# Performance work log

Measured on AMD Instinct MI355X. Metric: run time of the kernel, lower is better.

The kernel has to match this reference:

```python
import jax, jax.numpy as jnp
import numpy as np

N = 1200          # number of mentions in the block -> NxN SDP matrix
HID = 128         # MLP hidden width
RANK = 64         # Burer-Monteiro factor rank ~ sqrt(2N)
SDP_ITERS = 100   # fixed iteration budget (original caps at 50000)
BN_EPS = 1e-5


def setup_inputs() -> dict:
    key = jax.random.key(0)
    k = jax.random.split(key, 5)
    P = N * (N - 1) // 2
    x = jax.random.normal(k[0], (P, 39), jnp.float32)
    W1 = jax.random.normal(k[1], (39, HID), jnp.float32) * (1.0 / np.sqrt(39.0))
    b1 = jnp.zeros((HID,), jnp.float32)
    gamma = jnp.ones((HID,), jnp.float32)
    beta = jnp.zeros((HID,), jnp.float32)
    W2 = jax.random.normal(k[2], (HID, 1), jnp.float32) * (1.0 / np.sqrt(float(HID)))
    b2 = jnp.zeros((1,), jnp.float32)
    V0 = jax.random.normal(k[3], (N, RANK), jnp.float32)
    return {"x": x, "W1": W1, "b1": b1, "gamma": gamma, "beta": beta,
            "W2": W2, "b2": b2, "V0": V0}


def _forward(x, W1, b1, gamma, beta, W2, b2, V0):
    # MLPLayer: Linear -> BatchNorm (batch stats) -> ReLU -> Linear(->1)
    h = x @ W1 + b1                                   # [P, HID]
    mu = h.mean(axis=0)
    var = h.var(axis=0)
    h = (h - mu) * jax.lax.rsqrt(var + BN_EPS) * gamma + beta
    h = jax.nn.relu(h)
    w = (h @ W2 + b2).reshape(-1)                     # flat edge weights [P]

    # UncompressTransformLayer: flat upper-triangle -> symmetric NxN, zero diag
    iu, ju = jnp.triu_indices(N, k=1)
    A = jnp.zeros((N, N), w.dtype).at[iu, ju].set(w)
    W = A + A.T                                       # [N, N]

    # SDPLayer: max <W, X> s.t. X PSD, diag(X)=1, X>=0 via Burer-Monteiro
    # low-rank factorization with fixed-iteration projected gradient ascent.
    V = V0 / jnp.linalg.norm(V0, axis=1, keepdims=True)
    lr = 1.0 / (jnp.linalg.norm(W) + 1e-8)

    def step(V, _):
        V = V + lr * (W @ V)
        V = V / jnp.linalg.norm(V, axis=1, keepdims=True)
        return V, None

    V, _ = jax.lax.scan(step, V, None, length=SDP_ITERS)
    X = jnp.clip(V @ V.T, 0.0, 1.0)                   # output probabilities [N, N]
    return X


def reference(x, W1, b1, gamma, beta, W2, b2, V0):
    return _forward(x, W1, b1, gamma, beta, W2, b2, V0)
```

## Files before the change

kernel.cpp:

```cpp
#include <hip/hip_runtime.h>

#define NM 1200
#define PP 719400
#define HID 128
#define RANK 64
#define SDP_ITERS 100

#define OFF_S      0
#define OFF_SUMW2  1600
#define OFF_CVEC   1664
#define OFF_W1S    1792
#define OFF_WVEC   6912
#define OFF_WMAT   726400
#define OFF_VA     2166400
#define OFF_VB     2243200

__device__ __forceinline__ float wave_reduce_sum(float v) {
#pragma unroll
    for (int o = 32; o > 0; o >>= 1) v += __shfl_xor(v, o, 64);
    return v;
}

__global__ __launch_bounds__(256) void zero_kernel(float* __restrict__ ws, int n) {
    int i = blockIdx.x * 256 + threadIdx.x;
    if (i < n) ws[i] = 0.0f;
}

#define STATS_BLOCKS 1024
#define KT 40
__global__ __launch_bounds__(256) void stats_kernel(const float* __restrict__ x,
                                                    float* __restrict__ S) {
    __shared__ __align__(16) float tile[2][KT * 48];
    __shared__ float Sacc[48 * 48];
    const int tid = threadIdx.x;
    for (int i = tid; i < 48 * 48; i += 256) Sacc[i] = 0.f;
    for (int i = tid; i < 2 * KT * 8; i += 256) {
        int b = i / (KT * 8);
        int rem = i - b * (KT * 8);
        int r = rem >> 3, k = rem & 7;
        tile[b][r * 48 + 40 + k] = 0.f;
    }

    const int rpb = (PP + STATS_BLOCKS - 1) / STATS_BLOCKS;
    const int r0 = blockIdx.x * rpb;
    const int r1 = min(r0 + rpb, PP);

    const bool stg = tid < 200;
    const int sr = tid / 5;
    const int sc = (tid - sr * 5) * 8;
    float* const dA = &tile[0][sr * 48 + sc];
    float* const dB = &tile[1][sr * 48 + sc];
    const float* const srcb = x + (size_t)sr * 39 + sc;
    const bool tail = (sc == 32);

    const int z  = tid >> 6;
    const int ln = tid & 63;
    const int ty = ln >> 3, tx = ln & 7;

    float acc[6][6];
#pragma unroll
    for (int a = 0; a < 6; ++a)
#pragma unroll
        for (int b = 0; b < 6; ++b) acc[a][b] = 0.f;

    float v[8];
    {
        const float* s = srcb + (size_t)r0 * 39;
        const bool ok = stg && (r0 + sr < r1);
#pragma unroll
        for (int k = 0; k < 8; ++k) v[k] = 0.f;
        if (ok) {
#pragma unroll
            for (int k = 0; k < 7; ++k) v[k] = s[k];
            v[7] = tail ? 1.0f : s[7];
        }
    }
    if (stg) {
        *(float4*)dA       = make_float4(v[0], v[1], v[2], v[3]);
        *(float4*)(dA + 4) = make_float4(v[4], v[5], v[6], v[7]);
    }
    __syncthreads();

    int cur = 0;
    for (int t = r0; t < r1; t += KT) {
        const int tn = t + KT;
        const bool more = tn < r1;
        float vn[8];
        if (more) {
            const float* s = srcb + (size_t)tn * 39;
            const bool ok = stg && (tn + sr < r1);
#pragma unroll
            for (int k = 0; k < 8; ++k) vn[k] = 0.f;
            if (ok) {
#pragma unroll
                for (int k = 0; k < 7; ++k) vn[k] = s[k];
                vn[7] = tail ? 1.0f : s[7];
            }
        }
        const float* tb = tile[cur];
#pragma unroll 2
        for (int kk = 0; kk < KT / 4; ++kk) {
            const float* row = &tb[(kk * 4 + z) * 48];
            float2 a0 = *(const float2*)(row + ty * 6);
            float2 a1 = *(const float2*)(row + ty * 6 + 2);
            float2 a2 = *(const float2*)(row + ty * 6 + 4);
            float2 b0 = *(const float2*)(row + tx * 6);
            float2 b1 = *(const float2*)(row + tx * 6 + 2);
            float2 b2 = *(const float2*)(row + tx * 6 + 4);
            float av[6] = {a0.x, a0.y, a1.x, a1.y, a2.x, a2.y};
            float bv[6] = {b0.x, b0.y, b1.x, b1.y, b2.x, b2.y};
#pragma unroll
            for (int a = 0; a < 6; ++a)
#pragma unroll
                for (int b = 0; b < 6; ++b)
                    acc[a][b] = fmaf(av[a], bv[b], acc[a][b]);
        }
        if (more && stg) {
            float* d = cur ? dA : dB;
            *(float4*)d       = make_float4(vn[0], vn[1], vn[2], vn[3]);
            *(float4*)(d + 4) = make_float4(vn[4], vn[5], vn[6], vn[7]);
        }
        __syncthreads();
        cur ^= 1;
    }

#pragma unroll
    for (int a = 0; a < 6; ++a)
#pragma unroll
        for (int b = 0; b < 6; ++b)
            atomicAdd(&Sacc[(ty * 6 + a) * 48 + tx * 6 + b], acc[a][b]);
    __syncthreads();
    for (int i = tid; i < 1600; i += 256) {
        int r = i / 40, c = i - r * 40;
        atomicAdd(&S[i], Sacc[r * 48 + c]);
    }
}

__global__ __launch_bounds__(64) void bn_prep(const float* __restrict__ S,
                                              const float* __restrict__ W1,
                                              const float* __restrict__ gamma,
                                              const float* __restrict__ beta,
                                              float* __restrict__ W1s,
                                              float* __restrict__ cvec) {
    const int j = blockIdx.x;
    const int l = threadIdx.x;
    const float invP = 1.0f / (float)PP;
    float q = 0.f;
    for (int idx = l; idx < 39 * 39; idx += 64) {
        int a = idx / 39, b = idx - a * 39;
        q = fmaf(S[a * 40 + b], W1[a * HID + j] * W1[b * HID + j], q);
    }
    float s1 = (l < 39) ? (S[39 * 40 + l] * invP) * W1[l * HID + j] : 0.f;
    q = wave_reduce_sum(q);
    s1 = wave_reduce_sum(s1);
    float var = q * invP - s1 * s1;
    float scale = gamma[j] * (1.0f / sqrtf(var + 1e-5f));
    for (int a = l; a < 39; a += 64) W1s[a * HID + j] = W1[a * HID + j] * scale;
    if (l == 0) cvec[j] = -s1 * scale + beta[j];
}

__global__ __launch_bounds__(256) void mlp_kernel(const float* __restrict__ x,
                                                  const float* __restrict__ W1s,
                                                  const float* __restrict__ cvec,
                                                  const float* __restrict__ W2,
                                                  const float* __restrict__ b2,
                                                  float* __restrict__ w,
                                                  float* __restrict__ sumw2) {
    __shared__ float xt[256 * 39];
    __shared__ float red[4];
    const size_t base = (size_t)blockIdx.x * 256;
    {
        const size_t g0 = base * 39;
        const size_t gmax = (size_t)PP * 39;
        for (int idx = threadIdx.x; idx < 256 * 39; idx += 256) {
            size_t g = g0 + idx;
            xt[idx] = (g < gmax) ? x[g] : 0.f;
        }
    }
    __syncthreads();

    float xr[39];
    {
        const float* xrow = &xt[threadIdx.x * 39];
#pragma unroll
        for (int k = 0; k < 39; ++k) xr[k] = xrow[k];
    }

    float wacc = 0.f;
#pragma unroll 1
    for (int c = 0; c < 2; ++c) {
        float acc[64];
#pragma unroll
        for (int jj = 0; jj < 64; ++jj) acc[jj] = cvec[c * 64 + jj];
#pragma unroll 3
        for (int k = 0; k < 39; ++k) {
            const float xk = xr[k];
            const float* wrow = &W1s[k * HID + c * 64];
#pragma unroll
            for (int jj = 0; jj < 64; ++jj) acc[jj] = fmaf(xk, wrow[jj], acc[jj]);
        }
#pragma unroll
        for (int jj = 0; jj < 64; ++jj)
            wacc = fmaf(fmaxf(acc[jj], 0.f), W2[c * 64 + jj], wacc);
    }

    const size_t p = base + threadIdx.x;
    const float wv = wacc + b2[0];
    float sq = 0.f;
    if (p < (size_t)PP) { w[p] = wv; sq = wv * wv; }
    sq = wave_reduce_sum(sq);
    if ((threadIdx.x & 63) == 0) red[threadIdx.x >> 6] = sq;
    __syncthreads();
    if (threadIdx.x == 0) atomicAdd(sumw2, red[0] + red[1] + red[2] + red[3]);
}

__global__ __launch_bounds__(256) void buildW(const float* __restrict__ w,
                                              float* __restrict__ W) {
    __shared__ float tile[16][17];
    const int bi = blockIdx.y, bj = blockIdx.x;
    if (bi > bj) return;
    const int ty = threadIdx.x >> 4, tx = threadIdx.x & 15;
    const int i = bi * 16 + ty, j = bj * 16 + tx;
    float v = 0.f;
    if (i < j) {
        int p = i * (NM - 1) - (i * (i - 1)) / 2 + (j - i - 1);
        v = w[p];
    }
    tile[ty][tx] = v;
    __syncthreads();
    if (bi == bj) {
        float out = (i < j) ? v : ((i > j) ? tile[tx][ty] : 0.f);
        W[(size_t)i * NM + j] = out;
    } else {
        W[(size_t)i * NM + j] = v;
        W[(size_t)(bj * 16 + ty) * NM + (bi * 16 + tx)] = tile[tx][ty];
    }
}

__global__ __launch_bounds__(256) void v0norm(const float* __restrict__ V0,
                                              float* __restrict__ V) {
    const int i = blockIdx.x * 4 + (threadIdx.x >> 6);
    const int c = threadIdx.x & 63;
    float v = V0[(size_t)i * RANK + c];
    float s = wave_reduce_sum(v * v);
    V[(size_t)i * RANK + c] = v * (1.0f / sqrtf(s));
}

#define SDP_BLOCKS 240
#define ROWS_PB 5
#define VU 30

__device__ __forceinline__ void sdp_loadv(float* buf, const float* __restrict__ Vb, int tb) {
#pragma unroll
    for (int u = 0; u < VU; ++u) buf[u] = Vb[(size_t)(tb + u) * RANK];
}

__device__ __forceinline__ void sdp_fmav(float* acc, const float* buf,
                                         const float* __restrict__ Wb, int tb) {
#pragma unroll
    for (int u = 0; u < VU; ++u) {
#pragma unroll
        for (int r = 0; r < ROWS_PB; ++r)
            acc[r] = fmaf(Wb[(size_t)r * NM + tb + u], buf[u], acc[r]);
    }
}

__global__ __launch_bounds__(512) void sdp_step(const float* __restrict__ Vin,
                                                float* __restrict__ Vout,
                                                const float* __restrict__ W,
                                                const float* __restrict__ sumw2) {
    __shared__ float part[8][ROWS_PB][64];
    const int tid = threadIdx.x;
    const int c = tid & 63;
    const int wvid = tid >> 6;
    const int i0 = blockIdx.x * ROWS_PB;
    const int j0 = __builtin_amdgcn_readfirstlane(wvid * 150);

    const float* __restrict__ Wb = W + (size_t)i0 * NM + j0;
    const float* __restrict__ Vb = Vin + (size_t)j0 * RANK + c;

    float acc[ROWS_PB] = {0.f, 0.f, 0.f, 0.f, 0.f};
    float va[VU], vb[VU], vc[VU];

    sdp_loadv(va, Vb, 0);
    sdp_loadv(vb, Vb, 30);
    sdp_loadv(vc, Vb, 60);
    sdp_fmav(acc, va, Wb, 0);
    sdp_loadv(va, Vb, 90);
    sdp_fmav(acc, vb, Wb, 30);
    sdp_loadv(vb, Vb, 120);
    sdp_fmav(acc, vc, Wb, 60);
    sdp_fmav(acc, va, Wb, 90);
    sdp_fmav(acc, vb, Wb, 120);

#pragma unroll
    for (int r = 0; r < ROWS_PB; ++r) part[wvid][r][c] = acc[r];
    __syncthreads();

    if (tid < ROWS_PB * 64) {
        const int r2 = tid >> 6, c2 = tid & 63;
        float s = 0.f;
#pragma unroll
        for (int k = 0; k < 8; ++k) s += part[k][r2][c2];
        const float lr = 1.0f / (sqrtf(2.0f * sumw2[0]) + 1e-8f);
        float y = Vin[(size_t)(i0 + r2) * RANK + c2] + lr * s;
        float n = wave_reduce_sum(y * y);
        Vout[(size_t)(i0 + r2) * RANK + c2] = y * (1.0f / sqrtf(n));
    }
}

__global__ __launch_bounds__(256) void vvt_kernel(const float* __restrict__ V,
                                                  float* __restrict__ out) {
    const int bi = blockIdx.y, bj = blockIdx.x;
    if (bi > bj) return;
    __shared__ __align__(16) float Ti[64][132];
    __shared__ __align__(16) float Tj[64][132];
    const int tid = threadIdx.x;
    for (int idx = tid; idx < 128 * 64; idx += 256) {
        int row = idx >> 6, k = idx & 63;
        int gi = bi * 128 + row, gj = bj * 128 + row;
        Ti[k][row] = (gi < NM) ? V[(size_t)gi * RANK + k] : 0.f;
        Tj[k][row] = (gj < NM) ? V[(size_t)gj * RANK + k] : 0.f;
    }
    __syncthreads();
    const int ty = tid >> 4, tx = tid & 15;
    float acc[8][8];
#pragma unroll
    for (int a = 0; a < 8; ++a)
#pragma unroll
        for (int b = 0; b < 8; ++b) acc[a][b] = 0.f;
    for (int k = 0; k < 64; ++k) {
        float4 a0 = *(const float4*)&Ti[k][ty * 8];
        float4 a1 = *(const float4*)&Ti[k][ty * 8 + 4];
        float4 b0 = *(const float4*)&Tj[k][tx * 8];
        float4 b1 = *(const float4*)&Tj[k][tx * 8 + 4];
        float av[8] = {a0.x, a0.y, a0.z, a0.w, a1.x, a1.y, a1.z, a1.w};
        float bv[8] = {b0.x, b0.y, b0.z, b0.w, b1.x, b1.y, b1.z, b1.w};
#pragma unroll
        for (int a = 0; a < 8; ++a)
#pragma unroll
            for (int b = 0; b < 8; ++b)
                acc[a][b] = fmaf(av[a], bv[b], acc[a][b]);
    }
#pragma unroll
    for (int a = 0; a < 8; ++a) {
        int i = bi * 128 + 8 * ty + a;
        if (i >= NM) break;
        int jb = bj * 128 + 8 * tx;
        if (jb + 7 < NM) {
            float4 s0 = {fminf(fmaxf(acc[a][0], 0.f), 1.f), fminf(fmaxf(acc[a][1], 0.f), 1.f),
                         fminf(fmaxf(acc[a][2], 0.f), 1.f), fminf(fmaxf(acc[a][3], 0.f), 1.f)};
            float4 s1 = {fminf(fmaxf(acc[a][4], 0.f), 1.f), fminf(fmaxf(acc[a][5], 0.f), 1.f),
                         fminf(fmaxf(acc[a][6], 0.f), 1.f), fminf(fmaxf(acc[a][7], 0.f), 1.f)};
            *(float4*)&out[(size_t)i * NM + jb] = s0;
            *(float4*)&out[(size_t)i * NM + jb + 4] = s1;
        } else {
#pragma unroll
            for (int b = 0; b < 8; ++b) {
                int j = jb + b;
                if (j < NM) out[(size_t)i * NM + j] = fminf(fmaxf(acc[a][b], 0.f), 1.f);
            }
        }
    }
    if (bi != bj) {
#pragma unroll
        for (int b = 0; b < 8; ++b) {
            int j = bj * 128 + 8 * tx + b;
            if (j >= NM) break;
            int ib = bi * 128 + 8 * ty;
            if (ib + 7 < NM) {
                float4 s0 = {fminf(fmaxf(acc[0][b], 0.f), 1.f), fminf(fmaxf(acc[1][b], 0.f), 1.f),
                             fminf(fmaxf(acc[2][b], 0.f), 1.f), fminf(fmaxf(acc[3][b], 0.f), 1.f)};
                float4 s1 = {fminf(fmaxf(acc[4][b], 0.f), 1.f), fminf(fmaxf(acc[5][b], 0.f), 1.f),
                             fminf(fmaxf(acc[6][b], 0.f), 1.f), fminf(fmaxf(acc[7][b], 0.f), 1.f)};
                *(float4*)&out[(size_t)j * NM + ib] = s0;
                *(float4*)&out[(size_t)j * NM + ib + 4] = s1;
            } else {
#pragma unroll
                for (int a = 0; a < 8; ++a) {
                    int i = ib + a;
                    if (i < NM) out[(size_t)j * NM + i] = fminf(fmaxf(acc[a][b], 0.f), 1.f);
                }
            }
        }
    }
}

extern "C" void kernel_launch(void* const* d_in, const int* in_sizes, int n_in,
                              void* d_out, int out_size, void* d_ws, size_t ws_size,
                              hipStream_t stream) {
    const float* x     = (const float*)d_in[0];
    const float* W1    = (const float*)d_in[1];
    const float* gamma = (const float*)d_in[3];
    const float* beta  = (const float*)d_in[4];
    const float* W2    = (const float*)d_in[5];
    const float* b2    = (const float*)d_in[6];
    const float* V0    = (const float*)d_in[7];
    float* out = (float*)d_out;

    float* ws    = (float*)d_ws;
    float* S     = ws + OFF_S;
    float* sumw2 = ws + OFF_SUMW2;
    float* cvec  = ws + OFF_CVEC;
    float* W1s   = ws + OFF_W1S;
    float* wvec  = ws + OFF_WVEC;
    float* Wmat  = ws + OFF_WMAT;
    float* Va    = ws + OFF_VA;
    float* Vb    = ws + OFF_VB;

    zero_kernel<<<7, 256, 0, stream>>>(ws, OFF_W1S);
    stats_kernel<<<STATS_BLOCKS, 256, 0, stream>>>(x, S);
    bn_prep<<<HID, 64, 0, stream>>>(S, W1, gamma, beta, W1s, cvec);
    mlp_kernel<<<(PP + 255) / 256, 256, 0, stream>>>(x, W1s, cvec, W2, b2, wvec, sumw2);
    buildW<<<dim3(75, 75), 256, 0, stream>>>(wvec, Wmat);
    v0norm<<<NM / 4, 256, 0, stream>>>(V0, Va);
    for (int it = 0; it < SDP_ITERS; ++it) {
        const float* vin = (it & 1) ? Vb : Va;
        float* vout      = (it & 1) ? Va : Vb;
        sdp_step<<<SDP_BLOCKS, 512, 0, stream>>>(vin, vout, Wmat, sumw2);
    }
    vvt_kernel<<<dim3(10, 10), 256, 0, stream>>>(Va, out);
}
```

Before: 1.188 ms.

## Widen SDP step to 15 waves per block and split MLP hidden loop into quarters

The SDP iteration kernel now launches 960 threads per block, so each of 15 waves covers 80 columns instead of 150. The V loads use a shallower 16-wide double buffer, and the learning-rate load is hoisted to the top of the kernel. The intent is more memory-level parallelism and shorter per-wave latency chains in the 100 latency-bound iterations. The MLP kernel splits its 128 hidden units into four 32-wide chunks with a min-blocks hint of 4, to lower register pressure and raise occupancy, at the cost of re-reading x registers per chunk and a larger shared reduction in the SDP kernel.

```diff
diff --git a/kernel.cpp b/kernel.cpp
--- a/kernel.cpp
+++ b/kernel.cpp
@@ -159,13 +159,13 @@
     if (l == 0) cvec[j] = -s1 * scale + beta[j];
 }
 
-__global__ __launch_bounds__(256) void mlp_kernel(const float* __restrict__ x,
-                                                  const float* __restrict__ W1s,
-                                                  const float* __restrict__ cvec,
-                                                  const float* __restrict__ W2,
-                                                  const float* __restrict__ b2,
-                                                  float* __restrict__ w,
-                                                  float* __restrict__ sumw2) {
+__global__ __launch_bounds__(256, 4) void mlp_kernel(const float* __restrict__ x,
+                                                     const float* __restrict__ W1s,
+                                                     const float* __restrict__ cvec,
+                                                     const float* __restrict__ W2,
+                                                     const float* __restrict__ b2,
+                                                     float* __restrict__ w,
+                                                     float* __restrict__ sumw2) {
     __shared__ float xt[256 * 39];
     __shared__ float red[4];
     const size_t base = (size_t)blockIdx.x * 256;
@@ -181,27 +181,27 @@
 
     float xr[39];
     {
-        const float* xrow = &xt[threadIdx.x * 39];
+        const float* __restrict__ xrow = &xt[threadIdx.x * 39];
 #pragma unroll
         for (int k = 0; k < 39; ++k) xr[k] = xrow[k];
     }
 
     float wacc = 0.f;
 #pragma unroll 1
-    for (int c = 0; c < 2; ++c) {
-        float acc[64];
-#pragma unroll
-        for (int jj = 0; jj < 64; ++jj) acc[jj] = cvec[c * 64 + jj];
-#pragma unroll 3
+    for (int s = 0; s < 4; ++s) {
+        float acc[32];
+#pragma unroll
+        for (int jj = 0; jj < 32; ++jj) acc[jj] = cvec[s * 32 + jj];
+#pragma unroll
         for (int k = 0; k < 39; ++k) {
             const float xk = xr[k];
-            const float* wrow = &W1s[k * HID + c * 64];
-#pragma unroll
-            for (int jj = 0; jj < 64; ++jj) acc[jj] = fmaf(xk, wrow[jj], acc[jj]);
-        }
-#pragma unroll
-        for (int jj = 0; jj < 64; ++jj)
-            wacc = fmaf(fmaxf(acc[jj], 0.f), W2[c * 64 + jj], wacc);
+            const float* __restrict__ wrow = &W1s[k * HID + s * 32];
+#pragma unroll
+            for (int jj = 0; jj < 32; ++jj) acc[jj] = fmaf(xk, wrow[jj], acc[jj]);
+        }
+#pragma unroll
+        for (int jj = 0; jj < 32; ++jj)
+            wacc = fmaf(fmaxf(acc[jj], 0.f), W2[s * 32 + jj], wacc);
     }
 
     const size_t p = base + threadIdx.x;
@@ -248,50 +248,51 @@
 
 #define SDP_BLOCKS 240
 #define ROWS_PB 5
-#define VU 30
-
-__device__ __forceinline__ void sdp_loadv(float* buf, const float* __restrict__ Vb, int tb) {
-#pragma unroll
-    for (int u = 0; u < VU; ++u) buf[u] = Vb[(size_t)(tb + u) * RANK];
-}
-
-__device__ __forceinline__ void sdp_fmav(float* acc, const float* buf,
-                                         const float* __restrict__ Wb, int tb) {
-#pragma unroll
-    for (int u = 0; u < VU; ++u) {
+#define SDP_WAVES 15
+#define JCHUNK 80
+
+__device__ __forceinline__ void sdp_ld16(float* v, const float* __restrict__ Vb, int t0) {
+#pragma unroll
+    for (int u = 0; u < 16; ++u) v[u] = Vb[(size_t)(t0 + u) * RANK];
+}
+__device__ __forceinline__ void sdp_fma16(float* acc, const float* v,
+                                          const float* __restrict__ Wb, int t0) {
+#pragma unroll
+    for (int u = 0; u < 16; ++u) {
 #pragma unroll
         for (int r = 0; r < ROWS_PB; ++r)
-            acc[r] = fmaf(Wb[(size_t)r * NM + tb + u], buf[u], acc[r]);
-    }
-}
-
-__global__ __launch_bounds__(512) void sdp_step(const float* __restrict__ Vin,
+            acc[r] = fmaf(Wb[(size_t)r * NM + t0 + u], v[u], acc[r]);
+    }
+}
+
+__global__ __launch_bounds__(960) void sdp_step(const float* __restrict__ Vin,
                                                 float* __restrict__ Vout,
                                                 const float* __restrict__ W,
                                                 const float* __restrict__ sumw2) {
-    __shared__ float part[8][ROWS_PB][64];
+    __shared__ float part[SDP_WAVES][ROWS_PB][64];
     const int tid = threadIdx.x;
     const int c = tid & 63;
     const int wvid = tid >> 6;
     const int i0 = blockIdx.x * ROWS_PB;
-    const int j0 = __builtin_amdgcn_readfirstlane(wvid * 150);
+    const int j0 = __builtin_amdgcn_readfirstlane(wvid * JCHUNK);
+    const float lr = 1.0f / (sqrtf(2.0f * sumw2[0]) + 1e-8f);
 
     const float* __restrict__ Wb = W + (size_t)i0 * NM + j0;
     const float* __restrict__ Vb = Vin + (size_t)j0 * RANK + c;
 
     float acc[ROWS_PB] = {0.f, 0.f, 0.f, 0.f, 0.f};
-    float va[VU], vb[VU], vc[VU];
-
-    sdp_loadv(va, Vb, 0);
-    sdp_loadv(vb, Vb, 30);
-    sdp_loadv(vc, Vb, 60);
-    sdp_fmav(acc, va, Wb, 0);
-    sdp_loadv(va, Vb, 90);
-    sdp_fmav(acc, vb, Wb, 30);
-    sdp_loadv(vb, Vb, 120);
-    sdp_fmav(acc, vc, Wb, 60);
-    sdp_fmav(acc, va, Wb, 90);
-    sdp_fmav(acc, vb, Wb, 120);
+    float va[16], vb[16];
+
+    sdp_ld16(va, Vb, 0);
+    sdp_ld16(vb, Vb, 16);
+    sdp_fma16(acc, va, Wb, 0);
+    sdp_ld16(va, Vb, 32);
+    sdp_fma16(acc, vb, Wb, 16);
+    sdp_ld16(vb, Vb, 48);
+    sdp_fma16(acc, va, Wb, 32);
+    sdp_ld16(va, Vb, 64);
+    sdp_fma16(acc, vb, Wb, 48);
+    sdp_fma16(acc, va, Wb, 64);
 
 #pragma unroll
     for (int r = 0; r < ROWS_PB; ++r) part[wvid][r][c] = acc[r];
@@ -301,8 +302,7 @@
         const int r2 = tid >> 6, c2 = tid & 63;
         float s = 0.f;
 #pragma unroll
-        for (int k = 0; k < 8; ++k) s += part[k][r2][c2];
-        const float lr = 1.0f / (sqrtf(2.0f * sumw2[0]) + 1e-8f);
+        for (int k = 0; k < SDP_WAVES; ++k) s += part[k][r2][c2];
         float y = Vin[(size_t)(i0 + r2) * RANK + c2] + lr * s;
         float n = wave_reduce_sum(y * y);
         Vout[(size_t)(i0 + r2) * RANK + c2] = y * (1.0f / sqrtf(n));
@@ -417,7 +417,7 @@
     for (int it = 0; it < SDP_ITERS; ++it) {
         const float* vin = (it & 1) ? Vb : Va;
         float* vout      = (it & 1) ? Va : Vb;
-        sdp_step<<<SDP_BLOCKS, 512, 0, stream>>>(vin, vout, Wmat, sumw2);
+        sdp_step<<<SDP_BLOCKS, 960, 0, stream>>>(vin, vout, Wmat, sumw2);
     }
     vvt_kernel<<<dim3(10, 10), 256, 0, stream>>>(Va, out);
 }
```

Measured after the change: 1.149 ms. 3.3% less time.
